# Performance work log

Measured on AMD Instinct MI355X. Metric: run time of the kernel, lower is better.

## Reference

```python
import jax, jax.numpy as jnp
import numpy as np

N = 8192
IN_F = 256
OUT_F = 128
ALPHA = 0.2
NEG = -9000000000000000.0

def setup_inputs() -> dict:
    key = jax.random.key(0)
    k1, k2, k3, k4 = jax.random.split(key, 4)
    h = jax.random.normal(k1, (N, IN_F), dtype=jnp.float32)
    adj = jax.random.randint(k2, (N, N), 0, 2, dtype=jnp.int32)
    # xavier-uniform-like params
    limW = float(np.sqrt(6.0 / (IN_F + OUT_F)))
    W = jax.random.uniform(k3, (IN_F, OUT_F), minval=-limW, maxval=limW, dtype=jnp.float32)
    lima = float(np.sqrt(6.0 / (2 * OUT_F + 1)))
    a = jax.random.uniform(k4, (2 * OUT_F, 1), minval=-lima, maxval=lima, dtype=jnp.float32)
    return {"h": h, "adj": adj, "W": W, "a": a}

def reference(h, adj, W, a):
    Wh = h @ W  # [N, F]
    # e_ij = LeakyReLU(a1.Wh_i + a2.Wh_j) -- avoids [N,N,2F] intermediate
    a1 = a[:OUT_F, 0]  # [F]
    a2 = a[OUT_F:, 0]  # [F]
    f1 = Wh @ a1  # [N]
    f2 = Wh @ a2  # [N]
    e = jax.nn.leaky_relu(f1[:, None] + f2[None, :], negative_slope=ALPHA)  # [N,N]
    att = jnp.where(adj > 0, e, jnp.float32(NEG))
    att = jax.nn.softmax(att, axis=1)
    h_prime = att @ Wh  # [N, F]
    return h_prime
```

## Files before the change

kernel.cpp:

```cpp
#include <hip/hip_runtime.h>
#include <hip/hip_bf16.h>

#define N    8192
#define INF  256
#define OUTF 128
#define ALPHA 0.2f
#define JS   8
#define NTS  (N / JS / 32)

typedef __attribute__((ext_vector_type(8))) short bf16x8;
typedef __attribute__((ext_vector_type(4))) float f32x4;

__device__ __forceinline__ unsigned short f2bf(float x) {
    union { float f; unsigned u; } v; v.f = x;
    unsigned r = v.u + 0x7fff + ((v.u >> 16) & 1);
    return (unsigned short)(r >> 16);
}

__device__ __forceinline__ void gll16(const void* g, void* l) {
    __builtin_amdgcn_global_load_lds(
        (const __attribute__((address_space(1))) unsigned*)g,
        (__attribute__((address_space(3))) unsigned*)l, 16, 0, 0);
}

__global__ __launch_bounds__(256) void k01_prep(
        const int* __restrict__ adj, unsigned* __restrict__ bits,
        const float* __restrict__ h, const float* __restrict__ W,
        const float* __restrict__ a,
        unsigned short* __restrict__ WhTb, float* __restrict__ f1, float* __restrict__ f2) {
    __shared__ float hs[8][INF];
    const int t = threadIdx.x;

    if (blockIdx.x >= 1024) {
        const size_t g = (size_t)(blockIdx.x - 1024) * 256 + t;
        const int4* p = (const int4*)adj + g * 8;
        unsigned b = 0;
        #pragma unroll
        for (int u = 0; u < 8; ++u) {
            int4 v = p[u];
            b |= (v.x > 0 ? 1u : 0u) << (u * 4 + 0);
            b |= (v.y > 0 ? 1u : 0u) << (u * 4 + 1);
            b |= (v.z > 0 ? 1u : 0u) << (u * 4 + 2);
            b |= (v.w > 0 ? 1u : 0u) << (u * 4 + 3);
        }
        bits[g] = b;
        return;
    }

    const int i0 = blockIdx.x * 8;
    #pragma unroll
    for (int u = 0; u < 2; ++u) {
        int idx = u * 256 + t;
        int r   = idx >> 6;
        int kq  = idx & 63;
        *(float4*)&hs[r][kq * 4] = *(const float4*)(h + (size_t)(i0 + r) * INF + kq * 4);
    }
    __syncthreads();

    const int rg = t >> 5;
    const int ct = t & 31;
    float acc[4] = {0.f, 0.f, 0.f, 0.f};

    #pragma unroll 8
    for (int k = 0; k < INF; ++k) {
        float4 wv = *(const float4*)(W + (size_t)k * OUTF + ct * 4);
        float  hx = hs[rg][k];
        acc[0] += hx * wv.x; acc[1] += hx * wv.y;
        acc[2] += hx * wv.z; acc[3] += hx * wv.w;
    }

    const int r0 = i0 + rg;
    const int jb = r0 >> 5;
    const int jo = r0 & 31;
    #pragma unroll
    for (int cc = 0; cc < 4; ++cc)
        WhTb[(size_t)jb * 4096 + (ct * 4 + cc) * 32 + jo] = f2bf(acc[cc]);

    const float4 a1v = *(const float4*)(a + ct * 4);
    const float4 a2v = *(const float4*)(a + OUTF + ct * 4);
    float p1 = acc[0]*a1v.x + acc[1]*a1v.y + acc[2]*a1v.z + acc[3]*a1v.w;
    float p2 = acc[0]*a2v.x + acc[1]*a2v.y + acc[2]*a2v.z + acc[3]*a2v.w;
    #pragma unroll
    for (int off = 16; off > 0; off >>= 1) {
        p1 += __shfl_down(p1, off, 32);
        p2 += __shfl_down(p2, off, 32);
    }
    if (ct == 0) { f1[r0] = p1; f2[r0] = p2; }
}

__device__ __forceinline__ float pbit(float f1r, float fv, unsigned byte_,
                                      int u, float& dsum) {
    float s = f1r + fv;
    float e = fmaxf(s, ALPHA * s);
    float p = (byte_ & (1u << u)) ? __expf(e) : 0.f;
    dsum += p;
    return p;
}

#define VMB4 "s_waitcnt vmcnt(4)\n\ts_barrier"
#define VMB2 "s_waitcnt vmcnt(2)\n\ts_barrier"
#define VMB0 "s_waitcnt vmcnt(0)\n\ts_barrier"

#define K2STEP(WORD, O, JT, VMB, ISSUE)                                      \
    {                                                                        \
        if (ISSUE) {                                                         \
            const char* ws_ = (const char*)WhTb + (size_t)(tile0 + (JT) + 2) * 8192; \
            char* bd_ = (char*)&bsm[((O) + 2) & 3][0];                       \
            gll16(ws_ + tsw,        bd_ + wv * 1024);                        \
            gll16(ws_ + 4096 + tsw, bd_ + 4096 + wv * 1024);                 \
        }                                                                    \
        float4 F0_ = *(const float4*)&f2s[(JT) * 32 + quad * 8];             \
        float4 F1_ = *(const float4*)&f2s[(JT) * 32 + quad * 8 + 4];         \
        unsigned byte_ = ((WORD) >> (quad << 3)) & 0xffu;                    \
        float p0_ = pbit(f1r, F0_.x, byte_, 0, dsum);                        \
        float p1_ = pbit(f1r, F0_.y, byte_, 1, dsum);                        \
        float p2_ = pbit(f1r, F0_.z, byte_, 2, dsum);                        \
        float p3_ = pbit(f1r, F0_.w, byte_, 3, dsum);                        \
        float p4_ = pbit(f1r, F1_.x, byte_, 4, dsum);                        \
        float p5_ = pbit(f1r, F1_.y, byte_, 5, dsum);                        \
        float p6_ = pbit(f1r, F1_.z, byte_, 6, dsum);                        \
        float p7_ = pbit(f1r, F1_.w, byte_, 7, dsum);                        \
        union { __hip_bfloat162 hh[4]; bf16x8 v; } pk_;                      \
        pk_.hh[0] = __float22bfloat162_rn(make_float2(p0_, p1_));            \
        pk_.hh[1] = __float22bfloat162_rn(make_float2(p2_, p3_));            \
        pk_.hh[2] = __float22bfloat162_rn(make_float2(p4_, p5_));            \
        pk_.hh[3] = __float22bfloat162_rn(make_float2(p6_, p7_));            \
        bf16x8 afrag = pk_.v;                                                \
        asm volatile(VMB ::: "memory");                                      \
        const char* bb_ = (const char*)&bsm[(O)][0] + laneb2;                \
        bf16x8 b0_ = *(const bf16x8*)(bb_);                                  \
        bf16x8 b1_ = *(const bf16x8*)(bb_ + 1024);                           \
        bf16x8 b2_ = *(const bf16x8*)(bb_ + 2048);                           \
        bf16x8 b3_ = *(const bf16x8*)(bb_ + 3072);                           \
        bf16x8 b4_ = *(const bf16x8*)(bb_ + 4096);                           \
        bf16x8 b5_ = *(const bf16x8*)(bb_ + 5120);                           \
        bf16x8 b6_ = *(const bf16x8*)(bb_ + 6144);                           \
        bf16x8 b7_ = *(const bf16x8*)(bb_ + 7168);                           \
        acc0 = __builtin_amdgcn_mfma_f32_16x16x32_bf16(afrag, b0_, acc0, 0, 0, 0); \
        acc1 = __builtin_amdgcn_mfma_f32_16x16x32_bf16(afrag, b1_, acc1, 0, 0, 0); \
        acc2 = __builtin_amdgcn_mfma_f32_16x16x32_bf16(afrag, b2_, acc2, 0, 0, 0); \
        acc3 = __builtin_amdgcn_mfma_f32_16x16x32_bf16(afrag, b3_, acc3, 0, 0, 0); \
        acc4 = __builtin_amdgcn_mfma_f32_16x16x32_bf16(afrag, b4_, acc4, 0, 0, 0); \
        acc5 = __builtin_amdgcn_mfma_f32_16x16x32_bf16(afrag, b5_, acc5, 0, 0, 0); \
        acc6 = __builtin_amdgcn_mfma_f32_16x16x32_bf16(afrag, b6_, acc6, 0, 0, 0); \
        acc7 = __builtin_amdgcn_mfma_f32_16x16x32_bf16(afrag, b7_, acc7, 0, 0, 0); \
    }

__global__ __launch_bounds__(256, 4) void k2_attn(
        const unsigned* __restrict__ bits, const unsigned short* __restrict__ WhTb,
        const float* __restrict__ f1, const float* __restrict__ f2,
        float* __restrict__ num, float* __restrict__ den) {
    __shared__ unsigned short bsm[4][4096];
    __shared__ float f2s[1024];

    const int t    = threadIdx.x;
    const int wv   = t >> 6;
    const int ln   = t & 63;
    const int m16  = ln & 15;
    const int quad = ln >> 4;
    const int i0   = blockIdx.x * 64;
    const int s    = blockIdx.y;
    const int row  = i0 + wv * 16 + m16;
    const int tile0 = s * NTS;
    const int j0    = s * (N / JS);
    const int laneb2 = m16 * 64 + ((quad ^ ((m16 >> 1) & 3)) << 4);
    const int tsw = (t * 16) ^ (((t >> 3) & 3) << 4);

    *(float4*)&f2s[t * 4] = *(const float4*)(f2 + j0 + t * 4);
    {
        const char* ws0 = (const char*)WhTb + (size_t)tile0 * 8192;
        char* bd0 = (char*)&bsm[0][0];
        gll16(ws0 + tsw,        bd0 + wv * 1024);
        gll16(ws0 + 4096 + tsw, bd0 + 4096 + wv * 1024);
        const char* ws1 = ws0 + 8192;
        char* bd1 = (char*)&bsm[1][0];
        gll16(ws1 + tsw,        bd1 + wv * 1024);
        gll16(ws1 + 4096 + tsw, bd1 + 4096 + wv * 1024);
    }

    const float f1r = f1[row];
    const uint4* brow = (const uint4*)(bits + (size_t)row * 256 + tile0);

    f32x4 acc0 = {0.f,0.f,0.f,0.f}, acc1 = {0.f,0.f,0.f,0.f};
    f32x4 acc2 = {0.f,0.f,0.f,0.f}, acc3 = {0.f,0.f,0.f,0.f};
    f32x4 acc4 = {0.f,0.f,0.f,0.f}, acc5 = {0.f,0.f,0.f,0.f};
    f32x4 acc6 = {0.f,0.f,0.f,0.f}, acc7 = {0.f,0.f,0.f,0.f};
    float dsum = 0.f;

    uint4 bwc = brow[0];
    asm volatile("s_waitcnt lgkmcnt(0)\n\ts_barrier" ::: "memory");

    for (int g = 0; g < 7; ++g) {
        uint4 bwn = brow[g + 1];
        const int jtb = g * 4;
        K2STEP(bwc.x, 0, jtb + 0, VMB4, 1)
        K2STEP(bwc.y, 1, jtb + 1, VMB4, 1)
        K2STEP(bwc.z, 2, jtb + 2, VMB4, 1)
        K2STEP(bwc.w, 3, jtb + 3, VMB4, 1)
        bwc = bwn;
    }
    K2STEP(bwc.x, 0, 28, VMB4, 1)
    K2STEP(bwc.y, 1, 29, VMB4, 1)
    K2STEP(bwc.z, 2, 30, VMB2, 0)
    K2STEP(bwc.w, 3, 31, VMB0, 0)

    dsum += __shfl_xor(dsum, 16);
    dsum += __shfl_xor(dsum, 32);
    if (quad == 0) den[(size_t)s * N + row] = dsum;

    float* np = num + (size_t)s * N * OUTF;
    #pragma unroll
    for (int r = 0; r < 4; ++r) {
        const size_t orow = (size_t)(i0 + wv * 16 + quad * 4 + r) * OUTF;
        np[orow + 0 * 16 + m16] = acc0[r];
        np[orow + 1 * 16 + m16] = acc1[r];
        np[orow + 2 * 16 + m16] = acc2[r];
        np[orow + 3 * 16 + m16] = acc3[r];
        np[orow + 4 * 16 + m16] = acc4[r];
        np[orow + 5 * 16 + m16] = acc5[r];
        np[orow + 6 * 16 + m16] = acc6[r];
        np[orow + 7 * 16 + m16] = acc7[r];
    }
}

__global__ __launch_bounds__(256) void k3_combine(
        const float* __restrict__ num, const float* __restrict__ den,
        float* __restrict__ out) {
    const int idx = blockIdx.x * 256 + threadIdx.x;
    const int row = idx >> 5;
    const int c4  = (idx & 31) * 4;
    float4 ns = {0.f,0.f,0.f,0.f};
    float  ds = 0.f;
    #pragma unroll
    for (int s = 0; s < JS; ++s) {
        float4 nv = *(const float4*)(num + ((size_t)s * N + row) * OUTF + c4);
        ns.x += nv.x; ns.y += nv.y; ns.z += nv.z; ns.w += nv.w;
        ds += den[(size_t)s * N + row];
    }
    const float inv = 1.0f / ds;
    float4 o = {ns.x * inv, ns.y * inv, ns.z * inv, ns.w * inv};
    *(float4*)(out + (size_t)row * OUTF + c4) = o;
}

extern "C" void kernel_launch(void* const* d_in, const int* in_sizes, int n_in,
                              void* d_out, int out_size, void* d_ws, size_t ws_size,
                              hipStream_t stream) {
    const float* h   = (const float*)d_in[0];
    const int*   adj = (const int*)  d_in[1];
    const float* W   = (const float*)d_in[2];
    const float* a   = (const float*)d_in[3];
    float* out = (float*)d_out;

    unsigned short* WhTb = (unsigned short*)d_ws;
    float*    f1   = (float*)(WhTb + (size_t)N * OUTF);
    float*    f2   = f1 + N;
    float*    den  = f2 + N;
    unsigned* bits = (unsigned*)(den + (size_t)JS * N);
    float*    num  = (float*)(bits + (size_t)N * (N / 32));

    k01_prep  <<<1024 + (N / 32) * (N / 256), 256, 0, stream>>>(adj, bits, h, W, a, WhTb, f1, f2);
    k2_attn   <<<dim3(N / 64, JS), 256, 0, stream>>>(bits, WhTb, f1, f2, num, den);
    k3_combine<<<(N * OUTF / 4) / 256, 256, 0, stream>>>(num, den, out);
}
```

Before: 430.4 us.

## Fuse adjacency bit-packing into attention kernel, reading int adj directly

Removes the separate pass that packs the int32 adjacency matrix into bitmasks. The attention kernel now streams its slice of adj rows directly, one step ahead, and packs 8 entries per lane in registers. The vmcnt waits are widened to account for the extra in-flight loads. This saves writing and re-reading the bitmask buffer, but the attention kernel now reads 32 bytes per lane per tile from global memory, with strided row access that may coalesce less well.

```diff
diff --git a/kernel.cpp b/kernel.cpp
--- a/kernel.cpp
+++ b/kernel.cpp
@@ -23,29 +23,19 @@
         (__attribute__((address_space(3))) unsigned*)l, 16, 0, 0);
 }
 
-__global__ __launch_bounds__(256) void k01_prep(
-        const int* __restrict__ adj, unsigned* __restrict__ bits,
+__device__ __forceinline__ unsigned pack8(int4 a, int4 b) {
+    return (a.x > 0 ?   1u : 0u) | (a.y > 0 ?   2u : 0u)
+         | (a.z > 0 ?   4u : 0u) | (a.w > 0 ?   8u : 0u)
+         | (b.x > 0 ?  16u : 0u) | (b.y > 0 ?  32u : 0u)
+         | (b.z > 0 ?  64u : 0u) | (b.w > 0 ? 128u : 0u);
+}
+
+__global__ __launch_bounds__(256) void k1_prep(
         const float* __restrict__ h, const float* __restrict__ W,
         const float* __restrict__ a,
         unsigned short* __restrict__ WhTb, float* __restrict__ f1, float* __restrict__ f2) {
     __shared__ float hs[8][INF];
     const int t = threadIdx.x;
-
-    if (blockIdx.x >= 1024) {
-        const size_t g = (size_t)(blockIdx.x - 1024) * 256 + t;
-        const int4* p = (const int4*)adj + g * 8;
-        unsigned b = 0;
-        #pragma unroll
-        for (int u = 0; u < 8; ++u) {
-            int4 v = p[u];
-            b |= (v.x > 0 ? 1u : 0u) << (u * 4 + 0);
-            b |= (v.y > 0 ? 1u : 0u) << (u * 4 + 1);
-            b |= (v.z > 0 ? 1u : 0u) << (u * 4 + 2);
-            b |= (v.w > 0 ? 1u : 0u) << (u * 4 + 3);
-        }
-        bits[g] = b;
-        return;
-    }
 
     const int i0 = blockIdx.x * 8;
     #pragma unroll
@@ -97,13 +87,14 @@
     return p;
 }
 
-#define VMB4 "s_waitcnt vmcnt(4)\n\ts_barrier"
+#define VMB6 "s_waitcnt vmcnt(6)\n\ts_barrier"
 #define VMB2 "s_waitcnt vmcnt(2)\n\ts_barrier"
-#define VMB0 "s_waitcnt vmcnt(0)\n\ts_barrier"
-
-#define K2STEP(WORD, O, JT, VMB, ISSUE)                                      \
+
+#define K2STEP(O, JT, VMB, ISSG, ISSA)                                       \
     {                                                                        \
-        if (ISSUE) {                                                         \
+        int4 na_ = {}, nb_ = {};                                             \
+        if (ISSA) { na_ = arow[((JT) + 1) * 8]; nb_ = arow[((JT) + 1) * 8 + 1]; } \
+        if (ISSG) {                                                          \
             const char* ws_ = (const char*)WhTb + (size_t)(tile0 + (JT) + 2) * 8192; \
             char* bd_ = (char*)&bsm[((O) + 2) & 3][0];                       \
             gll16(ws_ + tsw,        bd_ + wv * 1024);                        \
@@ -111,7 +102,7 @@
         }                                                                    \
         float4 F0_ = *(const float4*)&f2s[(JT) * 32 + quad * 8];             \
         float4 F1_ = *(const float4*)&f2s[(JT) * 32 + quad * 8 + 4];         \
-        unsigned byte_ = ((WORD) >> (quad << 3)) & 0xffu;                    \
+        unsigned byte_ = byteC;                                              \
         float p0_ = pbit(f1r, F0_.x, byte_, 0, dsum);                        \
         float p1_ = pbit(f1r, F0_.y, byte_, 1, dsum);                        \
         float p2_ = pbit(f1r, F0_.z, byte_, 2, dsum);                        \
@@ -144,10 +135,11 @@
         acc5 = __builtin_amdgcn_mfma_f32_16x16x32_bf16(afrag, b5_, acc5, 0, 0, 0); \
         acc6 = __builtin_amdgcn_mfma_f32_16x16x32_bf16(afrag, b6_, acc6, 0, 0, 0); \
         acc7 = __builtin_amdgcn_mfma_f32_16x16x32_bf16(afrag, b7_, acc7, 0, 0, 0); \
+        if (ISSA) byteC = pack8(na_, nb_);                                   \
     }
 
 __global__ __launch_bounds__(256, 4) void k2_attn(
-        const unsigned* __restrict__ bits, const unsigned short* __restrict__ WhTb,
+        const int* __restrict__ adj, const unsigned short* __restrict__ WhTb,
         const float* __restrict__ f1, const float* __restrict__ f2,
         float* __restrict__ num, float* __restrict__ den) {
     __shared__ unsigned short bsm[4][4096];
@@ -166,6 +158,9 @@
     const int laneb2 = m16 * 64 + ((quad ^ ((m16 >> 1) & 3)) << 4);
     const int tsw = (t * 16) ^ (((t >> 3) & 3) << 4);
 
+    const int4* arow = (const int4*)(adj + (size_t)row * N + j0 + quad * 8);
+
+    int4 na0 = arow[0], nb0 = arow[1];
     *(float4*)&f2s[t * 4] = *(const float4*)(f2 + j0 + t * 4);
     {
         const char* ws0 = (const char*)WhTb + (size_t)tile0 * 8192;
@@ -179,7 +174,6 @@
     }
 
     const float f1r = f1[row];
-    const uint4* brow = (const uint4*)(bits + (size_t)row * 256 + tile0);
 
     f32x4 acc0 = {0.f,0.f,0.f,0.f}, acc1 = {0.f,0.f,0.f,0.f};
     f32x4 acc2 = {0.f,0.f,0.f,0.f}, acc3 = {0.f,0.f,0.f,0.f};
@@ -187,22 +181,20 @@
     f32x4 acc6 = {0.f,0.f,0.f,0.f}, acc7 = {0.f,0.f,0.f,0.f};
     float dsum = 0.f;
 
-    uint4 bwc = brow[0];
+    unsigned byteC = pack8(na0, nb0);
     asm volatile("s_waitcnt lgkmcnt(0)\n\ts_barrier" ::: "memory");
 
     for (int g = 0; g < 7; ++g) {
-        uint4 bwn = brow[g + 1];
         const int jtb = g * 4;
-        K2STEP(bwc.x, 0, jtb + 0, VMB4, 1)
-        K2STEP(bwc.y, 1, jtb + 1, VMB4, 1)
-        K2STEP(bwc.z, 2, jtb + 2, VMB4, 1)
-        K2STEP(bwc.w, 3, jtb + 3, VMB4, 1)
-        bwc = bwn;
-    }
-    K2STEP(bwc.x, 0, 28, VMB4, 1)
-    K2STEP(bwc.y, 1, 29, VMB4, 1)
-    K2STEP(bwc.z, 2, 30, VMB2, 0)
-    K2STEP(bwc.w, 3, 31, VMB0, 0)
+        K2STEP(0, jtb + 0, VMB6, 1, 1)
+        K2STEP(1, jtb + 1, VMB6, 1, 1)
+        K2STEP(2, jtb + 2, VMB6, 1, 1)
+        K2STEP(3, jtb + 3, VMB6, 1, 1)
+    }
+    K2STEP(0, 28, VMB6, 1, 1)
+    K2STEP(1, 29, VMB6, 1, 1)
+    K2STEP(2, 30, VMB6, 0, 1)
+    K2STEP(3, 31, VMB2, 0, 0)
 
     dsum += __shfl_xor(dsum, 16);
     dsum += __shfl_xor(dsum, 32);
@@ -255,10 +247,9 @@
     float*    f1   = (float*)(WhTb + (size_t)N * OUTF);
     float*    f2   = f1 + N;
     float*    den  = f2 + N;
-    unsigned* bits = (unsigned*)(den + (size_t)JS * N);
-    float*    num  = (float*)(bits + (size_t)N * (N / 32));
-
-    k01_prep  <<<1024 + (N / 32) * (N / 256), 256, 0, stream>>>(adj, bits, h, W, a, WhTb, f1, f2);
-    k2_attn   <<<dim3(N / 64, JS), 256, 0, stream>>>(bits, WhTb, f1, f2, num, den);
+    float*    num  = den + (size_t)JS * N;
+
+    k1_prep   <<<N / 8, 256, 0, stream>>>(h, W, a, WhTb, f1, f2);
+    k2_attn   <<<dim3(N / 64, JS), 256, 0, stream>>>(adj, WhTb, f1, f2, num, den);
     k3_combine<<<(N * OUTF / 4) / 256, 256, 0, stream>>>(num, den, out);
 }
```

After: 453.3 us. +5.3%, slower.

## Process two 16-row tiles per wave to reuse LDS B fragments

Applied to the files above, without the earlier changes.

Each wave in the attention kernel now handles 32 rows as two 16-row MFMA tiles that share the same B fragments read from LDS. This halves the LDS reads per MFMA. The block shrinks to 128 threads, so each wave issues four async global-to-LDS loads per tile, and the vmcnt waits are retuned to match. The cost is twice the accumulator registers (16 f32x4 per lane) and fewer waves per block, which may lower occupancy and latency hiding.

```diff
diff --git a/kernel.cpp b/kernel.cpp
--- a/kernel.cpp
+++ b/kernel.cpp
@@ -97,35 +97,52 @@
     return p;
 }
 
-#define VMB4 "s_waitcnt vmcnt(4)\n\ts_barrier"
-#define VMB2 "s_waitcnt vmcnt(2)\n\ts_barrier"
-#define VMB0 "s_waitcnt vmcnt(0)\n\ts_barrier"
-
-#define K2STEP(WORD, O, JT, VMB, ISSUE)                                      \
+#define VMB10 "s_waitcnt vmcnt(10)\n\ts_barrier"
+#define VMB8  "s_waitcnt vmcnt(8)\n\ts_barrier"
+#define VMB4  "s_waitcnt vmcnt(4)\n\ts_barrier"
+#define VMB0  "s_waitcnt vmcnt(0)\n\ts_barrier"
+
+#define K2STEP(WA, WB, O, JT, VMB, ISSG)                                     \
     {                                                                        \
-        if (ISSUE) {                                                         \
+        if (ISSG) {                                                          \
             const char* ws_ = (const char*)WhTb + (size_t)(tile0 + (JT) + 2) * 8192; \
-            char* bd_ = (char*)&bsm[((O) + 2) & 3][0];                       \
-            gll16(ws_ + tsw,        bd_ + wv * 1024);                        \
-            gll16(ws_ + 4096 + tsw, bd_ + 4096 + wv * 1024);                 \
+            char* bd_ = (char*)&bsm[((O) + 2) & 3][0] + wv * 4096;           \
+            const char* wsw_ = ws_ + wv * 4096 + lsw;                        \
+            gll16(wsw_ +    0, bd_ +    0);                                  \
+            gll16(wsw_ + 1024, bd_ + 1024);                                  \
+            gll16(wsw_ + 2048, bd_ + 2048);                                  \
+            gll16(wsw_ + 3072, bd_ + 3072);                                  \
         }                                                                    \
         float4 F0_ = *(const float4*)&f2s[(JT) * 32 + quad * 8];             \
         float4 F1_ = *(const float4*)&f2s[(JT) * 32 + quad * 8 + 4];         \
-        unsigned byte_ = ((WORD) >> (quad << 3)) & 0xffu;                    \
-        float p0_ = pbit(f1r, F0_.x, byte_, 0, dsum);                        \
-        float p1_ = pbit(f1r, F0_.y, byte_, 1, dsum);                        \
-        float p2_ = pbit(f1r, F0_.z, byte_, 2, dsum);                        \
-        float p3_ = pbit(f1r, F0_.w, byte_, 3, dsum);                        \
-        float p4_ = pbit(f1r, F1_.x, byte_, 4, dsum);                        \
-        float p5_ = pbit(f1r, F1_.y, byte_, 5, dsum);                        \
-        float p6_ = pbit(f1r, F1_.z, byte_, 6, dsum);                        \
-        float p7_ = pbit(f1r, F1_.w, byte_, 7, dsum);                        \
-        union { __hip_bfloat162 hh[4]; bf16x8 v; } pk_;                      \
-        pk_.hh[0] = __float22bfloat162_rn(make_float2(p0_, p1_));            \
-        pk_.hh[1] = __float22bfloat162_rn(make_float2(p2_, p3_));            \
-        pk_.hh[2] = __float22bfloat162_rn(make_float2(p4_, p5_));            \
-        pk_.hh[3] = __float22bfloat162_rn(make_float2(p6_, p7_));            \
-        bf16x8 afrag = pk_.v;                                                \
+        unsigned byA_ = ((WA) >> (quad << 3)) & 0xffu;                       \
+        unsigned byB_ = ((WB) >> (quad << 3)) & 0xffu;                       \
+        float a0_ = pbit(f1A, F0_.x, byA_, 0, dsA);                          \
+        float a1_ = pbit(f1A, F0_.y, byA_, 1, dsA);                          \
+        float a2_ = pbit(f1A, F0_.z, byA_, 2, dsA);                          \
+        float a3_ = pbit(f1A, F0_.w, byA_, 3, dsA);                          \
+        float a4_ = pbit(f1A, F1_.x, byA_, 4, dsA);                          \
+        float a5_ = pbit(f1A, F1_.y, byA_, 5, dsA);                          \
+        float a6_ = pbit(f1A, F1_.z, byA_, 6, dsA);                          \
+        float a7_ = pbit(f1A, F1_.w, byA_, 7, dsA);                          \
+        float c0_ = pbit(f1B, F0_.x, byB_, 0, dsB);                          \
+        float c1_ = pbit(f1B, F0_.y, byB_, 1, dsB);                          \
+        float c2_ = pbit(f1B, F0_.z, byB_, 2, dsB);                          \
+        float c3_ = pbit(f1B, F0_.w, byB_, 3, dsB);                          \
+        float c4_ = pbit(f1B, F1_.x, byB_, 4, dsB);                          \
+        float c5_ = pbit(f1B, F1_.y, byB_, 5, dsB);                          \
+        float c6_ = pbit(f1B, F1_.z, byB_, 6, dsB);                          \
+        float c7_ = pbit(f1B, F1_.w, byB_, 7, dsB);                          \
+        union { __hip_bfloat162 hh[4]; bf16x8 v; } pkA_, pkB_;               \
+        pkA_.hh[0] = __float22bfloat162_rn(make_float2(a0_, a1_));           \
+        pkA_.hh[1] = __float22bfloat162_rn(make_float2(a2_, a3_));           \
+        pkA_.hh[2] = __float22bfloat162_rn(make_float2(a4_, a5_));           \
+        pkA_.hh[3] = __float22bfloat162_rn(make_float2(a6_, a7_));           \
+        pkB_.hh[0] = __float22bfloat162_rn(make_float2(c0_, c1_));           \
+        pkB_.hh[1] = __float22bfloat162_rn(make_float2(c2_, c3_));           \
+        pkB_.hh[2] = __float22bfloat162_rn(make_float2(c4_, c5_));           \
+        pkB_.hh[3] = __float22bfloat162_rn(make_float2(c6_, c7_));           \
+        bf16x8 afA = pkA_.v, afB = pkB_.v;                                   \
         asm volatile(VMB ::: "memory");                                      \
         const char* bb_ = (const char*)&bsm[(O)][0] + laneb2;                \
         bf16x8 b0_ = *(const bf16x8*)(bb_);                                  \
@@ -136,17 +153,25 @@
         bf16x8 b5_ = *(const bf16x8*)(bb_ + 5120);                           \
         bf16x8 b6_ = *(const bf16x8*)(bb_ + 6144);                           \
         bf16x8 b7_ = *(const bf16x8*)(bb_ + 7168);                           \
-        acc0 = __builtin_amdgcn_mfma_f32_16x16x32_bf16(afrag, b0_, acc0, 0, 0, 0); \
-        acc1 = __builtin_amdgcn_mfma_f32_16x16x32_bf16(afrag, b1_, acc1, 0, 0, 0); \
-        acc2 = __builtin_amdgcn_mfma_f32_16x16x32_bf16(afrag, b2_, acc2, 0, 0, 0); \
-        acc3 = __builtin_amdgcn_mfma_f32_16x16x32_bf16(afrag, b3_, acc3, 0, 0, 0); \
-        acc4 = __builtin_amdgcn_mfma_f32_16x16x32_bf16(afrag, b4_, acc4, 0, 0, 0); \
-        acc5 = __builtin_amdgcn_mfma_f32_16x16x32_bf16(afrag, b5_, acc5, 0, 0, 0); \
-        acc6 = __builtin_amdgcn_mfma_f32_16x16x32_bf16(afrag, b6_, acc6, 0, 0, 0); \
-        acc7 = __builtin_amdgcn_mfma_f32_16x16x32_bf16(afrag, b7_, acc7, 0, 0, 0); \
-    }
-
-__global__ __launch_bounds__(256, 4) void k2_attn(
+        aA0 = __builtin_amdgcn_mfma_f32_16x16x32_bf16(afA, b0_, aA0, 0, 0, 0); \
+        aB0 = __builtin_amdgcn_mfma_f32_16x16x32_bf16(afB, b0_, aB0, 0, 0, 0); \
+        aA1 = __builtin_amdgcn_mfma_f32_16x16x32_bf16(afA, b1_, aA1, 0, 0, 0); \
+        aB1 = __builtin_amdgcn_mfma_f32_16x16x32_bf16(afB, b1_, aB1, 0, 0, 0); \
+        aA2 = __builtin_amdgcn_mfma_f32_16x16x32_bf16(afA, b2_, aA2, 0, 0, 0); \
+        aB2 = __builtin_amdgcn_mfma_f32_16x16x32_bf16(afB, b2_, aB2, 0, 0, 0); \
+        aA3 = __builtin_amdgcn_mfma_f32_16x16x32_bf16(afA, b3_, aA3, 0, 0, 0); \
+        aB3 = __builtin_amdgcn_mfma_f32_16x16x32_bf16(afB, b3_, aB3, 0, 0, 0); \
+        aA4 = __builtin_amdgcn_mfma_f32_16x16x32_bf16(afA, b4_, aA4, 0, 0, 0); \
+        aB4 = __builtin_amdgcn_mfma_f32_16x16x32_bf16(afB, b4_, aB4, 0, 0, 0); \
+        aA5 = __builtin_amdgcn_mfma_f32_16x16x32_bf16(afA, b5_, aA5, 0, 0, 0); \
+        aB5 = __builtin_amdgcn_mfma_f32_16x16x32_bf16(afB, b5_, aB5, 0, 0, 0); \
+        aA6 = __builtin_amdgcn_mfma_f32_16x16x32_bf16(afA, b6_, aA6, 0, 0, 0); \
+        aB6 = __builtin_amdgcn_mfma_f32_16x16x32_bf16(afB, b6_, aB6, 0, 0, 0); \
+        aA7 = __builtin_amdgcn_mfma_f32_16x16x32_bf16(afA, b7_, aA7, 0, 0, 0); \
+        aB7 = __builtin_amdgcn_mfma_f32_16x16x32_bf16(afB, b7_, aB7, 0, 0, 0); \
+    }
+
+__global__ __launch_bounds__(128, 2) void k2_attn(
         const unsigned* __restrict__ bits, const unsigned short* __restrict__ WhTb,
         const float* __restrict__ f1, const float* __restrict__ f2,
         float* __restrict__ num, float* __restrict__ den) {
@@ -160,66 +185,90 @@
     const int quad = ln >> 4;
     const int i0   = blockIdx.x * 64;
     const int s    = blockIdx.y;
-    const int row  = i0 + wv * 16 + m16;
+    const int rowA = i0 + wv * 32 + m16;
+    const int rowB = rowA + 16;
     const int tile0 = s * NTS;
     const int j0    = s * (N / JS);
     const int laneb2 = m16 * 64 + ((quad ^ ((m16 >> 1) & 3)) << 4);
-    const int tsw = (t * 16) ^ (((t >> 3) & 3) << 4);
-
-    *(float4*)&f2s[t * 4] = *(const float4*)(f2 + j0 + t * 4);
+    const int lsw = (ln * 16) ^ (((ln >> 3) & 3) << 4);
+
+    *(float4*)&f2s[t * 4]       = *(const float4*)(f2 + j0 + t * 4);
+    *(float4*)&f2s[512 + t * 4] = *(const float4*)(f2 + j0 + 512 + t * 4);
     {
-        const char* ws0 = (const char*)WhTb + (size_t)tile0 * 8192;
-        char* bd0 = (char*)&bsm[0][0];
-        gll16(ws0 + tsw,        bd0 + wv * 1024);
-        gll16(ws0 + 4096 + tsw, bd0 + 4096 + wv * 1024);
+        const char* ws0 = (const char*)WhTb + (size_t)tile0 * 8192 + wv * 4096 + lsw;
+        char* bd0 = (char*)&bsm[0][0] + wv * 4096;
+        gll16(ws0 +    0, bd0 +    0);
+        gll16(ws0 + 1024, bd0 + 1024);
+        gll16(ws0 + 2048, bd0 + 2048);
+        gll16(ws0 + 3072, bd0 + 3072);
         const char* ws1 = ws0 + 8192;
-        char* bd1 = (char*)&bsm[1][0];
-        gll16(ws1 + tsw,        bd1 + wv * 1024);
-        gll16(ws1 + 4096 + tsw, bd1 + 4096 + wv * 1024);
-    }
-
-    const float f1r = f1[row];
-    const uint4* brow = (const uint4*)(bits + (size_t)row * 256 + tile0);
-
-    f32x4 acc0 = {0.f,0.f,0.f,0.f}, acc1 = {0.f,0.f,0.f,0.f};
-    f32x4 acc2 = {0.f,0.f,0.f,0.f}, acc3 = {0.f,0.f,0.f,0.f};
-    f32x4 acc4 = {0.f,0.f,0.f,0.f}, acc5 = {0.f,0.f,0.f,0.f};
-    f32x4 acc6 = {0.f,0.f,0.f,0.f}, acc7 = {0.f,0.f,0.f,0.f};
-    float dsum = 0.f;
-
-    uint4 bwc = brow[0];
+        char* bd1 = (char*)&bsm[1][0] + wv * 4096;
+        gll16(ws1 +    0, bd1 +    0);
+        gll16(ws1 + 1024, bd1 + 1024);
+        gll16(ws1 + 2048, bd1 + 2048);
+        gll16(ws1 + 3072, bd1 + 3072);
+    }
+
+    const float f1A = f1[rowA];
+    const float f1B = f1[rowB];
+    const uint4* browA = (const uint4*)(bits + (size_t)rowA * 256 + tile0);
+    const uint4* browB = (const uint4*)(bits + (size_t)rowB * 256 + tile0);
+
+    f32x4 aA0 = {0.f,0.f,0.f,0.f}, aA1 = {0.f,0.f,0.f,0.f};
+    f32x4 aA2 = {0.f,0.f,0.f,0.f}, aA3 = {0.f,0.f,0.f,0.f};
+    f32x4 aA4 = {0.f,0.f,0.f,0.f}, aA5 = {0.f,0.f,0.f,0.f};
+    f32x4 aA6 = {0.f,0.f,0.f,0.f}, aA7 = {0.f,0.f,0.f,0.f};
+    f32x4 aB0 = {0.f,0.f,0.f,0.f}, aB1 = {0.f,0.f,0.f,0.f};
+    f32x4 aB2 = {0.f,0.f,0.f,0.f}, aB3 = {0.f,0.f,0.f,0.f};
+    f32x4 aB4 = {0.f,0.f,0.f,0.f}, aB5 = {0.f,0.f,0.f,0.f};
+    f32x4 aB6 = {0.f,0.f,0.f,0.f}, aB7 = {0.f,0.f,0.f,0.f};
+    float dsA = 0.f, dsB = 0.f;
+
+    uint4 bwcA = browA[0], bwcB = browB[0];
     asm volatile("s_waitcnt lgkmcnt(0)\n\ts_barrier" ::: "memory");
 
     for (int g = 0; g < 7; ++g) {
-        uint4 bwn = brow[g + 1];
+        uint4 bwnA = browA[g + 1], bwnB = browB[g + 1];
         const int jtb = g * 4;
-        K2STEP(bwc.x, 0, jtb + 0, VMB4, 1)
-        K2STEP(bwc.y, 1, jtb + 1, VMB4, 1)
-        K2STEP(bwc.z, 2, jtb + 2, VMB4, 1)
-        K2STEP(bwc.w, 3, jtb + 3, VMB4, 1)
-        bwc = bwn;
-    }
-    K2STEP(bwc.x, 0, 28, VMB4, 1)
-    K2STEP(bwc.y, 1, 29, VMB4, 1)
-    K2STEP(bwc.z, 2, 30, VMB2, 0)
-    K2STEP(bwc.w, 3, 31, VMB0, 0)
-
-    dsum += __shfl_xor(dsum, 16);
-    dsum += __shfl_xor(dsum, 32);
-    if (quad == 0) den[(size_t)s * N + row] = dsum;
+        K2STEP(bwcA.x, bwcB.x, 0, jtb + 0, VMB10, 1)
+        K2STEP(bwcA.y, bwcB.y, 1, jtb + 1, VMB10, 1)
+        K2STEP(bwcA.z, bwcB.z, 2, jtb + 2, VMB8, 1)
+        K2STEP(bwcA.w, bwcB.w, 3, jtb + 3, VMB8, 1)
+        bwcA = bwnA; bwcB = bwnB;
+    }
+    K2STEP(bwcA.x, bwcB.x, 0, 28, VMB8, 1)
+    K2STEP(bwcA.y, bwcB.y, 1, 29, VMB8, 1)
+    K2STEP(bwcA.z, bwcB.z, 2, 30, VMB4, 0)
+    K2STEP(bwcA.w, bwcB.w, 3, 31, VMB0, 0)
+
+    dsA += __shfl_xor(dsA, 16); dsA += __shfl_xor(dsA, 32);
+    dsB += __shfl_xor(dsB, 16); dsB += __shfl_xor(dsB, 32);
+    if (quad == 0) {
+        den[(size_t)s * N + rowA] = dsA;
+        den[(size_t)s * N + rowB] = dsB;
+    }
 
     float* np = num + (size_t)s * N * OUTF;
     #pragma unroll
     for (int r = 0; r < 4; ++r) {
-        const size_t orow = (size_t)(i0 + wv * 16 + quad * 4 + r) * OUTF;
-        np[orow + 0 * 16 + m16] = acc0[r];
-        np[orow + 1 * 16 + m16] = acc1[r];
-        np[orow + 2 * 16 + m16] = acc2[r];
-        np[orow + 3 * 16 + m16] = acc3[r];
-        np[orow + 4 * 16 + m16] = acc4[r];
-        np[orow + 5 * 16 + m16] = acc5[r];
-        np[orow + 6 * 16 + m16] = acc6[r];
-        np[orow + 7 * 16 + m16] = acc7[r];
+        const size_t orA = (size_t)(i0 + wv * 32 + quad * 4 + r) * OUTF;
+        np[orA + 0 * 16 + m16] = aA0[r];
+        np[orA + 1 * 16 + m16] = aA1[r];
+        np[orA + 2 * 16 + m16] = aA2[r];
+        np[orA + 3 * 16 + m16] = aA3[r];
+        np[orA + 4 * 16 + m16] = aA4[r];
+        np[orA + 5 * 16 + m16] = aA5[r];
+        np[orA + 6 * 16 + m16] = aA6[r];
+        np[orA + 7 * 16 + m16] = aA7[r];
+        const size_t orB = orA + (size_t)16 * OUTF;
+        np[orB + 0 * 16 + m16] = aB0[r];
+        np[orB + 1 * 16 + m16] = aB1[r];
+        np[orB + 2 * 16 + m16] = aB2[r];
+        np[orB + 3 * 16 + m16] = aB3[r];
+        np[orB + 4 * 16 + m16] = aB4[r];
+        np[orB + 5 * 16 + m16] = aB5[r];
+        np[orB + 6 * 16 + m16] = aB6[r];
+        np[orB + 7 * 16 + m16] = aB7[r];
     }
 }
 
@@ -259,6 +308,6 @@
     float*    num  = (float*)(bits + (size_t)N * (N / 32));
 
     k01_prep  <<<1024 + (N / 32) * (N / 256), 256, 0, stream>>>(adj, bits, h, W, a, WhTb, f1, f2);
-    k2_attn   <<<dim3(N / 64, JS), 256, 0, stream>>>(bits, WhTb, f1, f2, num, den);
+    k2_attn   <<<dim3(N / 64, JS), 128, 0, stream>>>(bits, WhTb, f1, f2, num, den);
     k3_combine<<<(N * OUTF / 4) / 256, 256, 0, stream>>>(num, den, out);
 }
```

Result: no change. 431.8 us (+0.3%).
